# Optimization experiments

Measured on AMD Instinct MI355X. Metric: run time of the kernel, lower is better.

The kernel has to match this reference:

```python
import jax, jax.numpy as jnp
import numpy as np

B, C, H, W = 4, 128, 64, 64


def setup_inputs() -> dict:
    key = jax.random.key(0)
    ks = jax.random.split(key, 7)
    s = 1.0 / np.sqrt(C)
    return {
        "x": jax.random.normal(ks[0], (B, C, H, W), dtype=jnp.float32),
        "Wq": jax.random.normal(ks[1], (C, C), dtype=jnp.float32) * s,
        "bq": jnp.zeros((C,), dtype=jnp.float32),
        "Wk": jax.random.normal(ks[2], (C, C), dtype=jnp.float32) * s,
        "bk": jnp.zeros((C,), dtype=jnp.float32),
        "Wv": jax.random.normal(ks[3], (C, C), dtype=jnp.float32) * s,
        "bv": jnp.zeros((C,), dtype=jnp.float32),
    }


def reference(x, Wq, bq, Wk, bk, Wv, bv):
    b, c, h, w = x.shape
    n = h * w
    scale = c ** (-0.5)
    # tokens: [B, N, C]
    xt = x.reshape(b, c, n).transpose(0, 2, 1)
    # 1x1 convs == per-token channel GEMMs (out[c'] = sum_c W[c',c] x[c] + b[c'])
    q = jnp.einsum("bnc,dc->bnd", xt, Wq) + bq  # [B, N, C]
    k = jnp.einsum("bnc,dc->bnd", xt, Wk) + bk  # [B, N, C]
    v = jnp.einsum("bnc,dc->bnd", xt, Wv) + bv  # [B, N, C]
    scores = jnp.einsum("bic,bjc->bij", q, k) * scale  # [B, N, N]
    attn = jax.nn.softmax(scores, axis=-1)
    out = jnp.einsum("bij,bjc->bic", attn, v)  # [B, N, C]
    return out.transpose(0, 2, 1).reshape(b, c, h, w)
```

## Files before the change

### kernel.cpp

```cpp
#include <hip/hip_runtime.h>
#include <hip/hip_bf16.h>


#define BATCH 4
#define CH    128
#define NTOK  4096
#define TK    64
#define SCALE 0.08838834764831845f
#define LOG2E 1.4426950408889634f
#define MFIX  16.0f
#define PSTR  72

typedef __attribute__((ext_vector_type(8)))  short short8;
typedef __attribute__((ext_vector_type(4)))  float f32x4;
typedef __attribute__((ext_vector_type(16))) float f32x16;

static __device__ __forceinline__ unsigned short f2bf(float f) {
    __hip_bfloat16 h = (__hip_bfloat16)f;
    return *(const unsigned short*)&h;
}

__global__ __launch_bounds__(256) void convert_w_kernel(
    const float* __restrict__ Wq, const float* __restrict__ Wk,
    const float* __restrict__ Wv, unsigned short* __restrict__ wb)
{
    const int idx = (blockIdx.x * 256 + threadIdx.x) * 4;
    const float* srcs[3] = {Wq, Wk, Wv};
    #pragma unroll
    for (int m = 0; m < 3; ++m) {
        float4 v = *(const float4*)(srcs[m] + idx);
        unsigned short o[4] = {f2bf(v.x), f2bf(v.y), f2bf(v.z), f2bf(v.w)};
        *(uint2*)(wb + (size_t)m * CH * CH + idx) = *(const uint2*)o;
    }
}

__global__ __launch_bounds__(256) void proj_mfma_kernel(
    const float* __restrict__ x,
    const unsigned short* __restrict__ wqb, const unsigned short* __restrict__ wkb,
    const unsigned short* __restrict__ wvb,
    const float* __restrict__ bq, const float* __restrict__ bk,
    const float* __restrict__ bv,
    unsigned short* __restrict__ q_ws, unsigned short* __restrict__ k_ws,
    unsigned short* __restrict__ vt_ws)
{
    __shared__ __align__(16) unsigned short XsT[64 * CH];

    const int t    = threadIdx.x;
    const int w    = t >> 6;
    const int lane = t & 63;
    const int quad = lane >> 4;
    const int c16  = lane & 15;
    const int n0   = blockIdx.x * 64;
    const int b    = blockIdx.y;
    const float* xb = x + (size_t)b * CH * NTOK;

    {
        const int tok = lane;
        #pragma unroll
        for (int cc = 0; cc < 4; ++cc) {
            const int cb = 32 * w + 8 * cc;
            unsigned short tmp[8];
            #pragma unroll
            for (int j = 0; j < 8; ++j)
                tmp[j] = f2bf(xb[(size_t)(cb + j) * NTOK + n0 + tok]);
            const int phys = ((cb >> 3) ^ (tok & 15));
            *(short8*)&XsT[tok * CH + phys * 8] = *(const short8*)tmp;
        }
    }
    __syncthreads();

    short8 xa[4];
    #pragma unroll
    for (int ks = 0; ks < 4; ++ks)
        xa[ks] = *(const short8*)&XsT[(16 * w + c16) * CH + (((4 * ks + quad) ^ c16) << 3)];

    #pragma unroll
    for (int nt = 0; nt < 8; ++nt) {
        f32x4 aq = (f32x4){0.f, 0.f, 0.f, 0.f};
        f32x4 ak = (f32x4){0.f, 0.f, 0.f, 0.f};
        const unsigned short* wqr = wqb + (16 * nt + c16) * CH;
        const unsigned short* wkr = wkb + (16 * nt + c16) * CH;
        #pragma unroll
        for (int ks = 0; ks < 4; ++ks) {
            const short8 bqf = *(const short8*)(wqr + 32 * ks + 8 * quad);
            const short8 bkf = *(const short8*)(wkr + 32 * ks + 8 * quad);
            aq = __builtin_amdgcn_mfma_f32_16x16x32_bf16(xa[ks], bqf, aq, 0, 0, 0);
            ak = __builtin_amdgcn_mfma_f32_16x16x32_bf16(xa[ks], bkf, ak, 0, 0, 0);
        }
        const float bqv = bq[16 * nt + c16];
        const float bkv = bk[16 * nt + c16];
        #pragma unroll
        for (int r = 0; r < 4; ++r) {
            const int n = n0 + 16 * w + quad * 4 + r;
            const size_t o = ((size_t)b * NTOK + n) * CH + 16 * nt + c16;
            q_ws[o] = f2bf((aq[r] + bqv) * (SCALE * LOG2E));
            k_ws[o] = f2bf(ak[r] + bkv);
        }
    }

    short8 wva[2][4];
    float  bvv[2][4];
    #pragma unroll
    for (int mt = 0; mt < 2; ++mt) {
        const int crow16 = 16 * (2 * w + mt);
        #pragma unroll
        for (int ks = 0; ks < 4; ++ks)
            wva[mt][ks] = *(const short8*)&wvb[(crow16 + c16) * CH + 32 * ks + 8 * quad];
        #pragma unroll
        for (int r = 0; r < 4; ++r)
            bvv[mt][r] = bv[crow16 + quad * 4 + r];
    }
    #pragma unroll
    for (int nt = 0; nt < 4; ++nt) {
        short8 xbf[4];
        #pragma unroll
        for (int ks = 0; ks < 4; ++ks)
            xbf[ks] = *(const short8*)&XsT[(16 * nt + c16) * CH + (((4 * ks + quad) ^ c16) << 3)];
        #pragma unroll
        for (int mt = 0; mt < 2; ++mt) {
            f32x4 acc = (f32x4){0.f, 0.f, 0.f, 0.f};
            #pragma unroll
            for (int ks = 0; ks < 4; ++ks)
                acc = __builtin_amdgcn_mfma_f32_16x16x32_bf16(wva[mt][ks], xbf[ks], acc, 0, 0, 0);
            #pragma unroll
            for (int r = 0; r < 4; ++r) {
                const int crow = 16 * (2 * w + mt) + quad * 4 + r;
                vt_ws[((size_t)b * CH + crow) * NTOK + n0 + 16 * nt + c16] =
                    f2bf(acc[r] + bvv[mt][r]);
            }
        }
    }
}

template <int SPLIT>
__global__ __launch_bounds__(256, 2) void flash_attn_mfma(
    const unsigned short* __restrict__ q_ws,
    const unsigned short* __restrict__ k_ws,
    const unsigned short* __restrict__ vt_ws,
    float* __restrict__ out,
    float* __restrict__ Op, float* __restrict__ l_p)
{
    __shared__ __align__(16) unsigned short KsU[TK * CH];
    __shared__ __align__(16) unsigned short VtU[CH * TK];
    __shared__ __align__(16) unsigned short PlU[4 * 32 * PSTR];

    const int t    = threadIdx.x;
    const int w    = t >> 6;
    const int lane = t & 63;
    const int half = lane >> 5;
    const int l32  = lane & 31;
    const int jc   = blockIdx.y;
    const int b    = blockIdx.z;
    const int n0   = blockIdx.x * 128;
    const int jbeg = jc * (NTOK / SPLIT);
    const int jend = jbeg + (NTOK / SPLIT);

    short8 qa[8];
    {
        const unsigned short* qrow = q_ws + ((size_t)b * NTOK + n0 + 32 * w + l32) * CH;
        #pragma unroll
        for (int ks = 0; ks < 8; ++ks)
            qa[ks] = *(const short8*)(qrow + ks * 16 + half * 8);
    }

    f32x16 Oa[4];
    #pragma unroll
    for (int ct = 0; ct < 4; ++ct) Oa[ct] = (f32x16)(0.0f);
    f32x16 La = (f32x16)(0.0f);

    const unsigned short* kg = k_ws  + (size_t)b * NTOK * CH;
    const unsigned short* vg = vt_ws + (size_t)b * CH * NTOK;
    const short8 ones8 = (short8)(short)0x3F80;
    unsigned short* Pw = &PlU[w * 32 * PSTR];

    for (int j0 = jbeg; j0 < jend; j0 += TK) {
        __syncthreads();

        {
            const int rl = lane >> 4, u = lane & 15;
            #pragma unroll
            for (int ci = 0; ci < 4; ++ci) {
                const int row = 16 * w + 4 * ci + rl;
                const int g   = u ^ (row & 15);
                const unsigned short* src = kg + (size_t)(j0 + row) * CH + g * 8;
                __builtin_amdgcn_global_load_lds(
                    (const __attribute__((address_space(1))) void*)src,
                    (__attribute__((address_space(3))) void*)&KsU[(16 * w + 4 * ci) * CH],
                    16, 0, 0);
            }
        }
        {
            const int cl = lane >> 3, u = lane & 7;
            #pragma unroll
            for (int ci = 0; ci < 4; ++ci) {
                const int c = 32 * w + 8 * ci + cl;
                const int g = u ^ (c & 7);
                const unsigned short* src = vg + (size_t)c * NTOK + j0 + g * 8;
                __builtin_amdgcn_global_load_lds(
                    (const __attribute__((address_space(1))) void*)src,
                    (__attribute__((address_space(3))) void*)&VtU[(32 * w + 8 * ci) * TK],
                    16, 0, 0);
            }
        }
        __syncthreads();

        f32x16 s0 = (f32x16)(-MFIX);
        f32x16 s1 = (f32x16)(-MFIX);
        #pragma unroll
        for (int ks = 0; ks < 8; ++ks) {
            const int ph = (2 * ks + half) ^ (l32 & 15);
            const short8 kf0 = *(const short8*)&KsU[l32 * CH + ph * 8];
            const short8 kf1 = *(const short8*)&KsU[(32 + l32) * CH + ph * 8];
            s0 = __builtin_amdgcn_mfma_f32_32x32x16_bf16(qa[ks], kf0, s0, 0, 0, 0);
            s1 = __builtin_amdgcn_mfma_f32_32x32x16_bf16(qa[ks], kf1, s1, 0, 0, 0);
        }

        #pragma unroll
        for (int reg = 0; reg < 16; ++reg) {
            const int row = (reg & 3) + 8 * (reg >> 2) + 4 * half;
            Pw[row * PSTR + l32]      = f2bf(exp2f(s0[reg]));
            Pw[row * PSTR + 32 + l32] = f2bf(exp2f(s1[reg]));
        }
        __threadfence_block();

        #pragma unroll
        for (int ks2 = 0; ks2 < 4; ++ks2) {
            const short8 pa = *(const short8*)&Pw[l32 * PSTR + ks2 * 16 + half * 8];
            #pragma unroll
            for (int ct = 0; ct < 4; ++ct) {
                const int ch = ct * 32 + l32;
                const int ph = (2 * ks2 + half) ^ (ch & 7);
                const short8 vf = *(const short8*)&VtU[ch * TK + ph * 8];
                Oa[ct] = __builtin_amdgcn_mfma_f32_32x32x16_bf16(pa, vf, Oa[ct], 0, 0, 0);
            }
            La = __builtin_amdgcn_mfma_f32_32x32x16_bf16(pa, ones8, La, 0, 0, 0);
        }
    }

    if constexpr (SPLIT == 1) {
        #pragma unroll
        for (int reg = 0; reg < 16; ++reg) {
            const int row = (reg & 3) + 8 * (reg >> 2) + 4 * half;
            const int n = n0 + 32 * w + row;
            const float inv = 1.0f / La[reg];
            #pragma unroll
            for (int ct = 0; ct < 4; ++ct)
                out[((size_t)b * CH + ct * 32 + l32) * NTOK + n] = Oa[ct][reg] * inv;
        }
    } else {
        const size_t chunk = (size_t)(b * SPLIT + jc);
        #pragma unroll
        for (int reg = 0; reg < 16; ++reg) {
            const int row = (reg & 3) + 8 * (reg >> 2) + 4 * half;
            const int n = n0 + 32 * w + row;
            const size_t base = (chunk * NTOK + n) * CH;
            #pragma unroll
            for (int ct = 0; ct < 4; ++ct)
                Op[base + ct * 32 + l32] = Oa[ct][reg];
            if (l32 == 0) l_p[chunk * NTOK + n] = La[reg];
        }
    }
}

template <int SPLIT>
__global__ __launch_bounds__(256) void combine_kernel(
    const float* __restrict__ Op, const float* __restrict__ l_p,
    float* __restrict__ out)
{
    const int t  = threadIdx.x;
    const int cg = t & 31;
    const int r8 = t >> 5;
    const int n0 = blockIdx.x * 64;
    const int b  = blockIdx.y;

    for (int it = 0; it < 8; ++it) {
        const int n = n0 + it * 8 + r8;
        float den = 0.f;
        float4 acc = make_float4(0.f, 0.f, 0.f, 0.f);
        #pragma unroll
        for (int j = 0; j < SPLIT; ++j) {
            const size_t chunk = (size_t)(b * SPLIT + j);
            den += l_p[chunk * NTOK + n];
            const float4 o = *(const float4*)&Op[(chunk * NTOK + n) * CH + cg * 4];
            acc.x += o.x; acc.y += o.y; acc.z += o.z; acc.w += o.w;
        }
        const float inv = 1.0f / den;
        out[((size_t)b * CH + cg * 4 + 0) * NTOK + n] = acc.x * inv;
        out[((size_t)b * CH + cg * 4 + 1) * NTOK + n] = acc.y * inv;
        out[((size_t)b * CH + cg * 4 + 2) * NTOK + n] = acc.z * inv;
        out[((size_t)b * CH + cg * 4 + 3) * NTOK + n] = acc.w * inv;
    }
}

extern "C" void kernel_launch(void* const* d_in, const int* in_sizes, int n_in,
                              void* d_out, int out_size, void* d_ws, size_t ws_size,
                              hipStream_t stream) {
    const float* x  = (const float*)d_in[0];
    const float* Wq = (const float*)d_in[1];
    const float* bq = (const float*)d_in[2];
    const float* Wk = (const float*)d_in[3];
    const float* bk = (const float*)d_in[4];
    const float* Wv = (const float*)d_in[5];
    const float* bv = (const float*)d_in[6];
    float* out = (float*)d_out;

    const size_t QKV = (size_t)BATCH * NTOK * CH;
    unsigned short* q_ws  = (unsigned short*)d_ws;
    unsigned short* k_ws  = q_ws + QKV;
    unsigned short* vt_ws = k_ws + QKV;
    unsigned short* wb    = vt_ws + QKV;
    float* Op = (float*)(wb + 3 * CH * CH);

    const size_t baseBytes = 3 * QKV * 2 + 3 * CH * CH * 2;
    auto needBytes = [&](size_t S) {
        return baseBytes + S * BATCH * NTOK * (size_t)(CH * 4 + 4);
    };

    convert_w_kernel<<<CH * CH / (256 * 4), 256, 0, stream>>>(Wq, Wk, Wv, wb);

    dim3 gp(NTOK / 64, BATCH);
    proj_mfma_kernel<<<gp, 256, 0, stream>>>(x, wb, wb + CH * CH, wb + 2 * CH * CH,
                                             bq, bk, bv, q_ws, k_ws, vt_ws);

    if (ws_size >= needBytes(8)) {
        float* l_p = Op + (size_t)8 * BATCH * NTOK * CH;
        dim3 ga(NTOK / 128, 8, BATCH);
        flash_attn_mfma<8><<<ga, 256, 0, stream>>>(q_ws, k_ws, vt_ws, out, Op, l_p);
        dim3 gc(NTOK / 64, BATCH);
        combine_kernel<8><<<gc, 256, 0, stream>>>(Op, l_p, out);
    } else if (ws_size >= needBytes(4)) {
        float* l_p = Op + (size_t)4 * BATCH * NTOK * CH;
        dim3 ga(NTOK / 128, 4, BATCH);
        flash_attn_mfma<4><<<ga, 256, 0, stream>>>(q_ws, k_ws, vt_ws, out, Op, l_p);
        dim3 gc(NTOK / 64, BATCH);
        combine_kernel<4><<<gc, 256, 0, stream>>>(Op, l_p, out);
    } else {
        dim3 ga(NTOK / 128, 1, BATCH);
        flash_attn_mfma<1><<<ga, 256, 0, stream>>>(q_ws, k_ws, vt_ws, out,
                                                   nullptr, nullptr);
    }
}
```

Before: 146.2 us.

## Stage projection outputs in LDS for coalesced stores and retune attention occupancy

The projection kernel now writes Q, K and V^T tiles into padded shared-memory staging buffers and then stores them to global memory as 16-byte vectors, replacing scattered 2-byte stores. The P-tile padding stride in the attention kernel drops from 72 to 66 to change LDS bank mapping and footprint. The launch-bounds minimum for the attention kernel rises to 3 blocks per CU, and the combine kernel uses half as many tokens per block so more blocks launch. These changes add LDS use and barriers to the projection kernel and may cause register spills in the attention kernel, or misaligned vector LDS accesses if P rows are read as 16-byte vectors with the new stride.

Result: slower. 247.6 us (+69.3%).

```diff
diff --git a/kernel.cpp b/kernel.cpp
--- a/kernel.cpp
+++ b/kernel.cpp
@@ -9,7 +9,7 @@
 #define SCALE 0.08838834764831845f
 #define LOG2E 1.4426950408889634f
 #define MFIX  16.0f
-#define PSTR  72
+#define PSTR  66
 
 typedef __attribute__((ext_vector_type(8)))  short short8;
 typedef __attribute__((ext_vector_type(4)))  float f32x4;
@@ -44,6 +44,8 @@
     unsigned short* __restrict__ vt_ws)
 {
     __shared__ __align__(16) unsigned short XsT[64 * CH];
+    __shared__ __align__(16) unsigned short StgA[8448];
+    __shared__ __align__(16) unsigned short StgB[8448];
 
     const int t    = threadIdx.x;
     const int w    = t >> 6;
@@ -91,49 +93,62 @@
         const float bkv = bk[16 * nt + c16];
         #pragma unroll
         for (int r = 0; r < 4; ++r) {
-            const int n = n0 + 16 * w + quad * 4 + r;
-            const size_t o = ((size_t)b * NTOK + n) * CH + 16 * nt + c16;
-            q_ws[o] = f2bf((aq[r] + bqv) * (SCALE * LOG2E));
-            k_ws[o] = f2bf(ak[r] + bkv);
-        }
-    }
-
-    short8 wva[2][4];
-    float  bvv[2][4];
+            const int row = 16 * w + 4 * quad + r;
+            StgA[row * 130 + 16 * nt + c16] = f2bf((aq[r] + bqv) * (SCALE * LOG2E));
+            StgB[row * 130 + 16 * nt + c16] = f2bf(ak[r] + bkv);
+        }
+    }
+    __syncthreads();
+
+    {
+        const int row = t >> 2, seg = t & 3;
+        unsigned short* qdst = q_ws + ((size_t)b * NTOK + n0 + row) * CH + seg * 32;
+        unsigned short* kdst = k_ws + ((size_t)b * NTOK + n0 + row) * CH + seg * 32;
+        #pragma unroll
+        for (int k = 0; k < 4; ++k) {
+            *(short8*)(qdst + k * 8) = *(const short8*)&StgA[row * 130 + seg * 32 + k * 8];
+            *(short8*)(kdst + k * 8) = *(const short8*)&StgB[row * 130 + seg * 32 + k * 8];
+        }
+    }
+    __syncthreads();
+
     #pragma unroll
     for (int mt = 0; mt < 2; ++mt) {
+        short8 wva[4];
         const int crow16 = 16 * (2 * w + mt);
         #pragma unroll
         for (int ks = 0; ks < 4; ++ks)
-            wva[mt][ks] = *(const short8*)&wvb[(crow16 + c16) * CH + 32 * ks + 8 * quad];
-        #pragma unroll
-        for (int r = 0; r < 4; ++r)
-            bvv[mt][r] = bv[crow16 + quad * 4 + r];
-    }
-    #pragma unroll
-    for (int nt = 0; nt < 4; ++nt) {
-        short8 xbf[4];
-        #pragma unroll
-        for (int ks = 0; ks < 4; ++ks)
-            xbf[ks] = *(const short8*)&XsT[(16 * nt + c16) * CH + (((4 * ks + quad) ^ c16) << 3)];
-        #pragma unroll
-        for (int mt = 0; mt < 2; ++mt) {
+            wva[ks] = *(const short8*)&wvb[(crow16 + c16) * CH + 32 * ks + 8 * quad];
+        #pragma unroll
+        for (int nt = 0; nt < 4; ++nt) {
+            short8 xbf[4];
+            #pragma unroll
+            for (int ks = 0; ks < 4; ++ks)
+                xbf[ks] = *(const short8*)&XsT[(16 * nt + c16) * CH + (((4 * ks + quad) ^ c16) << 3)];
             f32x4 acc = (f32x4){0.f, 0.f, 0.f, 0.f};
             #pragma unroll
             for (int ks = 0; ks < 4; ++ks)
-                acc = __builtin_amdgcn_mfma_f32_16x16x32_bf16(wva[mt][ks], xbf[ks], acc, 0, 0, 0);
+                acc = __builtin_amdgcn_mfma_f32_16x16x32_bf16(wva[ks], xbf[ks], acc, 0, 0, 0);
             #pragma unroll
             for (int r = 0; r < 4; ++r) {
-                const int crow = 16 * (2 * w + mt) + quad * 4 + r;
-                vt_ws[((size_t)b * CH + crow) * NTOK + n0 + 16 * nt + c16] =
-                    f2bf(acc[r] + bvv[mt][r]);
+                const int crow = crow16 + 4 * quad + r;
+                StgA[crow * 66 + 16 * nt + c16] = f2bf(acc[r] + bv[crow]);
             }
         }
     }
+    __syncthreads();
+
+    {
+        const int c = t >> 1, th = t & 1;
+        unsigned short* vdst = vt_ws + ((size_t)b * CH + c) * NTOK + n0 + th * 32;
+        #pragma unroll
+        for (int k = 0; k < 4; ++k)
+            *(short8*)(vdst + k * 8) = *(const short8*)&StgA[c * 66 + th * 32 + k * 8];
+    }
 }
 
 template <int SPLIT>
-__global__ __launch_bounds__(256, 2) void flash_attn_mfma(
+__global__ __launch_bounds__(256, 3) void flash_attn_mfma(
     const unsigned short* __restrict__ q_ws,
     const unsigned short* __restrict__ k_ws,
     const unsigned short* __restrict__ vt_ws,
@@ -270,10 +285,10 @@
     const int t  = threadIdx.x;
     const int cg = t & 31;
     const int r8 = t >> 5;
-    const int n0 = blockIdx.x * 64;
+    const int n0 = blockIdx.x * 32;
     const int b  = blockIdx.y;
 
-    for (int it = 0; it < 8; ++it) {
+    for (int it = 0; it < 4; ++it) {
         const int n = n0 + it * 8 + r8;
         float den = 0.f;
         float4 acc = make_float4(0.f, 0.f, 0.f, 0.f);
@@ -326,13 +341,13 @@
         float* l_p = Op + (size_t)8 * BATCH * NTOK * CH;
         dim3 ga(NTOK / 128, 8, BATCH);
         flash_attn_mfma<8><<<ga, 256, 0, stream>>>(q_ws, k_ws, vt_ws, out, Op, l_p);
-        dim3 gc(NTOK / 64, BATCH);
+        dim3 gc(NTOK / 32, BATCH);
         combine_kernel<8><<<gc, 256, 0, stream>>>(Op, l_p, out);
     } else if (ws_size >= needBytes(4)) {
         float* l_p = Op + (size_t)4 * BATCH * NTOK * CH;
         dim3 ga(NTOK / 128, 4, BATCH);
         flash_attn_mfma<4><<<ga, 256, 0, stream>>>(q_ws, k_ws, vt_ws, out, Op, l_p);
-        dim3 gc(NTOK / 64, BATCH);
+        dim3 gc(NTOK / 32, BATCH);
         combine_kernel<4><<<gc, 256, 0, stream>>>(Op, l_p, out);
     } else {
         dim3 ga(NTOK / 128, 1, BATCH);
```
